# Kernel tuning notes

Measured on AMD Instinct MI355X. Metric: run time of the kernel, lower is better.

The kernel has to match this reference:

```python
import jax, jax.numpy as jnp
import numpy as np

B, T, F = 256, 2048, 20
H_NODES = 256


def _heaviside(x):
    # smooth heaviside approx used throughout the original module
    return (jnp.tanh(10.0 * x) + 1.0) * 0.5


def _evap(wu, wl, wd, pet):
    h = _heaviside
    et1 = h(wu - pet) * pet + h(pet - wu) * wu
    rp = h(pet - et1) * (pet - et1)  # h(-(pet-et1))*0 term vanishes
    et22 = h(rp - wl) * wl + h(wl - rp) * rp
    et2 = h(rp) * et22
    et33 = h(rp - et2 - wd) * wd + h(wd - (rp - et2)) * (rp - et2)
    et3 = h(rp - et2) * et33
    return et1, et2, et3


def _runoff(wu, wl, wd, p, wum, wlm, wdm, b, c):
    wum = wum * 19.9 + 0.1
    wlm = wlm * 30.0 + 60.0
    wdm = wdm * 60.0 + 60.0
    c = c * 0.19 + 0.01
    b = b * 0.3 + 0.1
    w_total = wum + wlm + wdm
    s = c * (wu / w_total) ** 2 + b * (wl / w_total) ** 2
    return _heaviside(p - s) * (p - s)


def _partition(runoff, k1, k2, k3):
    k1 = k1 * 0.69 + 0.01
    k2 = k2 * 0.69 + 0.01
    k3 = k3 * 0.89 + 0.01
    sr = k1 * runoff
    itf = k2 * (runoff - sr)
    bf = k3 * (runoff - sr - itf)
    return sr, itf, bf


def setup_inputs() -> dict:
    key = jax.random.key(0)
    ks = jax.random.split(key, 7)
    u = lambda k, shp: jax.random.uniform(k, shp, jnp.float32, -0.05, 0.05)
    inputs = jax.random.uniform(ks[0], (B, T, F), jnp.float32)
    return {
        "inputs": inputs,
        "w1": u(ks[1], (15, H_NODES)),
        "b1": jnp.zeros((H_NODES,), jnp.float32),
        "w2": u(ks[2], (H_NODES, 64)),
        "b2": jnp.zeros((64,), jnp.float32),
        "w3": u(ks[3], (64, 8)),
        "b3": jnp.zeros((8,), jnp.float32),
    }


def reference(inputs, w1, b1, w2, b2, w3, b3):
    pet = inputs[..., 0:1]
    tmean = inputs[..., 1:2]
    p = inputs[..., 2:3]
    attrs = inputs[..., 5:]  # [B,T,15]

    # static-attribute -> physical-parameter MLP
    h1 = jnp.tanh(attrs @ w1 + b1)
    h2 = jnp.tanh(h1 @ w2 + b2)
    params = jax.nn.sigmoid(h2 @ w3 + b3)  # [B,T,8]

    xs = jnp.concatenate([pet, p, tmean, params], axis=-1)  # [B,T,11]

    def step(state, x):
        wu, wl, wd = state[:, 0:1], state[:, 1:2], state[:, 2:3]
        pet_t, p_t = x[:, 0:1], x[:, 1:2]
        et1, et2, et3 = _evap(wu, wl, wd, pet_t)
        clip = lambda d: jnp.clip(d, -1e5, 1e5)
        wu_n = wu + clip(p_t - et1)
        wl_n = wl + clip(p_t - et1 - et2)
        wd_n = wd + clip(p_t - et1 - et2 - et3)
        ns = jnp.concatenate([wu_n, wl_n, wd_n], axis=1)  # [B,3]
        return ns, ns

    init = jnp.zeros((inputs.shape[0], 3), inputs.dtype)
    _, outs = jax.lax.scan(step, init, jnp.swapaxes(xs, 0, 1))  # [T,B,3]
    outputs = jnp.swapaxes(outs, 0, 1)  # [B,T,3]

    wu, wl, wd = outputs[..., 0:1], outputs[..., 1:2], outputs[..., 2:3]
    wum, wlm, wdm = params[..., 0:1], params[..., 1:2], params[..., 2:3]
    b, c = params[..., 3:4], params[..., 4:5]
    k1, k2, k3 = params[..., 5:6], params[..., 6:7], params[..., 7:8]

    et1, et2, et3 = _evap(wu, wl, wd, pet)
    # NOTE: original call() swaps (wl,wd) and (wlm,wdm) here - kept faithful
    runoff = _runoff(wu, wd, wl, p, wum, wdm, wlm, b, c)
    sr, itf, bf = _partition(runoff, k1, k2, k3)
    total_q = sr + itf * 0.5 + bf * 0.25  # flow routing
    return total_q  # [B,T,1]
```

## Files before the change

### kernel.cpp

```cpp
#include <hip/hip_runtime.h>

#define B_ 256
#define T_ 2048
#define F_ 20
#define NT (B_*T_)
#define CH 16
#define NCH (T_/CH)

typedef __bf16 bf16x8 __attribute__((ext_vector_type(8)));
typedef float  f32x4  __attribute__((ext_vector_type(4)));

__device__ __forceinline__ float ex2(float x){ return __builtin_amdgcn_exp2f(x); }
__device__ __forceinline__ float rcpf_(float x){ return __builtin_amdgcn_rcpf(x); }

#define K10F 28.853900817779268f
#define K1F   2.8853900817779268f
#define LOG2E 1.4426950408889634f

__device__ __forceinline__ float hside(float x){ return 1.0f - rcpf_(ex2(K10F*x) + 1.0f); }
__device__ __forceinline__ float tanh_f(float z){ return 1.0f - 2.0f*rcpf_(ex2(K1F*z) + 1.0f); }
__device__ __forceinline__ float sigmoid_f(float z){ return rcpf_(1.0f + ex2(-LOG2E*z)); }

__device__ __forceinline__ void lds_barrier(){
  asm volatile("s_waitcnt lgkmcnt(0)" ::: "memory");
  __builtin_amdgcn_s_barrier();
  asm volatile("" ::: "memory");
}


__global__ __launch_bounds__(256) void prep_kernel(const float* __restrict__ in,
                                                   float* __restrict__ ws){
  int r = blockIdx.x*256 + threadIdx.x;
  if (r >= NT) return;
  int b = r & (B_-1);
  int t = r >> 8;
  const float* src = in + ((size_t)b*T_ + t)*F_;
  ((float2*)ws)[r] = make_float2(src[0], src[2]);
}

__global__ __launch_bounds__(512) void fused_kernel(const float* __restrict__ in,
    const float* __restrict__ w1, const float* __restrict__ b1,
    const float* __restrict__ w2, const float* __restrict__ b2,
    const float* __restrict__ w3, const float* __restrict__ b3,
    float* __restrict__ ws){
  extern __shared__ char sm[];
  float* pk4 = ws + 4*(size_t)NT;

  if (blockIdx.x < 4) {
    asm volatile("s_setprio 3");
    const float2* pp2 = (const float2*)ws;
    float* wuT = ws + 2*(size_t)NT;
    float* wdT = ws + 3*(size_t)NT;
    float*  d1L = (float*)sm;
    float*  bsQ = (float*)(sm + 8192);
    float2* rhL = (float2*)(sm + 24576);
    float2* qbL = (float2*)(sm + 40960);

    int tid = threadIdx.x;
    int wv = tid >> 6, lane = tid & 63;
    int boff = blockIdx.x * 64;

    float wu = 0.0f, wl = 0.0f, wd = 0.0f;
    float2 buf[2][8];

    if (wv == 0){
      #pragma unroll
      for (int g = 0; g < 2; ++g)
        #pragma unroll
        for (int i = 0; i < 8; ++i)
          buf[g][i] = pp2[(g*8 + i)*B_ + boff + lane];
    }

    for (int it = 0; it < NCH + 3; ++it){
      if (wv == 0){
        if (it < NCH){
          int c = it, par = c & 1;
          #pragma unroll
          for (int g = 0; g < 2; ++g){
            #pragma unroll
            for (int i = 0; i < 8; ++i){
              int s = g*8 + i;
              float pet = buf[g][i].x, p = buf[g][i].y;
              float d  = wu - pet;
              float r1 = rcpf_(ex2(K10F*d) + 1.0f);
              float d1 = -d*r1;
              float base = (p - pet) + d1;
              wu += base;
              wuT[(c*CH + s)*B_ + boff + lane] = wu;
              d1L[par*(CH*64) + s*64 + lane] = d1;
              bsQ[(c&3)*(CH*64) + s*64 + lane] = base;
            }
            int cn = (c + 1 < NCH) ? c + 1 : c;
            #pragma unroll
            for (int i = 0; i < 8; ++i)
              buf[g][i] = pp2[(cn*CH + g*8 + i)*B_ + boff + lane];
          }
        }
      } else if (wv == 1){
        if (it >= 1 && it <= NCH){
          int c = it - 1, par = c & 1;
          #pragma unroll
          for (int s = 0; s < CH; ++s){
            float d1 = d1L[par*(CH*64) + s*64 + lane];
            float r2 = rcpf_(ex2(K10F*d1) + 1.0f);
            float rp = fmaf(-d1, r2, d1);
            float hrp = 1.0f - rcpf_(ex2(K10F*rp) + 1.0f);
            rhL[par*(CH*64) + s*64 + lane] = make_float2(rp, hrp);
          }
        }
      } else if (wv == 2){
        if (it >= 2 && it <= NCH + 1){
          int c = it - 2, par = c & 1;
          #pragma unroll
          for (int s = 0; s < CH; ++s){
            float2 rh  = rhL[par*(CH*64) + s*64 + lane];
            float base = bsQ[(c&3)*(CH*64) + s*64 + lane];
            float d2   = rh.x - wl;
            float r    = rcpf_(ex2(K10F*d2) + 1.0f);
            float et22 = fmaf(d2, r, wl);
            float et2  = rh.y * et22;
            float b2v  = base - et2;
            wl += b2v;
            qbL[par*(CH*64) + s*64 + lane] = make_float2(rh.x - et2, b2v);
          }
        }
      } else if (wv == 3){
        if (it >= 3){
          int c = it - 3, par = c & 1;
          #pragma unroll
          for (int s = 0; s < CH; ++s){
            float2 qb  = qbL[par*(CH*64) + s*64 + lane];
            float hqv  = 1.0f - rcpf_(ex2(K10F*qb.x) + 1.0f);
            float d3   = qb.x - wd;
            float r    = rcpf_(ex2(K10F*d3) + 1.0f);
            float et33 = fmaf(d3, r, wd);
            float et3  = hqv * et33;
            wd += qb.y - et3;
            wdT[(c*CH + s)*B_ + boff + lane] = wd;
          }
        }
      }
      lds_barrier();
    }
    return;
  }

  __bf16* w1f   = (__bf16*)sm;
  __bf16* w2f   = (__bf16*)(sm + 8192);
  float*  b1s   = (float*)(sm + 24576);
  float*  b2s   = (float*)(sm + 25600);
  float*  b3s   = (float*)(sm + 25856);
  __bf16* hbufA = (__bf16*)(sm + 25888);

  int tid  = threadIdx.x;
  int lane = tid & 63;
  int wv   = tid >> 6;
  int m    = lane & 15;
  int q    = lane >> 4;
  int r0   = (blockIdx.x - 4)*256 + wv*32;

  bf16x8 a1[2];
  #pragma unroll
  for (int u = 0; u < 2; ++u){
    int rowA = r0 + u*16 + m;
    int bA = rowA & (B_-1), tA = rowA >> 8;
    const float* ap = in + ((size_t)bA*T_ + tA)*F_ + 5;
    #pragma unroll
    for (int j = 0; j < 8; ++j){
      int k = q*8 + j;
      a1[u][j] = (__bf16)((k < 15) ? ap[k] : 0.0f);
    }
  }
  bf16x8 w3h[2], w3l[2];
  #pragma unroll
  for (int kb = 0; kb < 2; ++kb){
    #pragma unroll
    for (int j = 0; j < 8; ++j){
      float v = (m < 8) ? w3[(kb*32 + q*8 + j)*8 + m] : 0.0f;
      __bf16 hi = (__bf16)v;
      w3h[kb][j] = hi;
      w3l[kb][j] = (__bf16)(v - (float)hi);
    }
  }

  ((float4*)sm)[tid] = make_float4(0.0f, 0.0f, 0.0f, 0.0f);
  __syncthreads();
  for (int idx = tid; idx < 15*256; idx += 512){
    int k = idx >> 8, n = idx & 255;
    int ct = n >> 4;
    int l  = ((k>>3)*16) + (n & 15);
    int j  = k & 7;
    w1f[(ct*32 + l)*8 + j] = (__bf16)w1[idx];
  }
  for (int idx = tid; idx < 8192; idx += 512){
    int kk = idx >> 6, n = idx & 63;
    int kb2 = kk >> 5;
    int lq  = (kk >> 3) & 3;
    int j   = kk & 7;
    int ct  = n >> 4;
    int l   = lq*16 + (n & 15);
    w2f[((kb2*4 + ct)*64 + l)*8 + j] = (__bf16)w2[kk*64 + n];
  }
  if (tid < 256) b1s[tid] = b1[tid];
  if (tid < 64)  b2s[tid] = b2[tid];
  if (tid < 8)   b3s[tid] = b3[tid];
  __syncthreads();

  f32x4 zero4 = {0.0f, 0.0f, 0.0f, 0.0f};
  bf16x8 zero8;
  #pragma unroll
  for (int j = 0; j < 8; ++j) zero8[j] = (__bf16)0.0f;

  __bf16* hb = hbufA + wv*2304;
  f32x4 acc2[2][4] = {{zero4, zero4, zero4, zero4},
                      {zero4, zero4, zero4, zero4}};

  #pragma unroll
  for (int pc = 0; pc < 2; ++pc){
    if (pc == 1){
      __syncthreads();
      for (int idx = tid; idx < 8192; idx += 512){
        int kk = idx >> 6, n = idx & 63;
        int kb2 = kk >> 5;
        int lq  = (kk >> 3) & 3;
        int j   = kk & 7;
        int ct  = n >> 4;
        int l   = lq*16 + (n & 15);
        w2f[((kb2*4 + ct)*64 + l)*8 + j] = (__bf16)w2[(128 + kk)*64 + n];
      }
      __syncthreads();
    }
    #pragma unroll
    for (int ph = 0; ph < 2; ++ph){
      int p = pc*2 + ph;
      #pragma unroll
      for (int c4 = 0; c4 < 4; ++c4){
        int ct = p*4 + c4;
        bf16x8 bw = zero8;
        if (lane < 32) bw = *(const bf16x8*)&w1f[(ct*32 + lane)*8];
        int f = c4*16 + m;
        float bb = b1s[p*64 + f];
        #pragma unroll
        for (int u = 0; u < 2; ++u){
          f32x4 c1 = __builtin_amdgcn_mfma_f32_16x16x32_bf16(a1[u], bw, zero4, 0, 0, 0);
          #pragma unroll
          for (int i = 0; i < 4; ++i){
            float h = tanh_f(c1[i] + bb);
            hb[(u*16 + q*4 + i)*72 + f] = (__bf16)h;
          }
        }
      }
      #pragma unroll
      for (int kb = 0; kb < 2; ++kb){
        bf16x8 a2_0 = *(const bf16x8*)&hb[ m      *72 + kb*32 + q*8];
        bf16x8 a2_1 = *(const bf16x8*)&hb[(16 + m)*72 + kb*32 + q*8];
        #pragma unroll
        for (int ct = 0; ct < 4; ++ct){
          bf16x8 bw2 = *(const bf16x8*)&w2f[(((ph*2 + kb)*4 + ct)*64 + lane)*8];
          acc2[0][ct] = __builtin_amdgcn_mfma_f32_16x16x32_bf16(a2_0, bw2, acc2[0][ct], 0, 0, 0);
          acc2[1][ct] = __builtin_amdgcn_mfma_f32_16x16x32_bf16(a2_1, bw2, acc2[1][ct], 0, 0, 0);
        }
      }
    }
  }

  #pragma unroll
  for (int ct = 0; ct < 4; ++ct){
    int f = ct*16 + m;
    float bb = b2s[f];
    #pragma unroll
    for (int u = 0; u < 2; ++u)
      #pragma unroll
      for (int i = 0; i < 4; ++i){
        float h = tanh_f(acc2[u][ct][i] + bb);
        hb[(u*16 + q*4 + i)*72 + f] = (__bf16)h;
      }
  }

  f32x4 acc3[2] = {zero4, zero4};
  #pragma unroll
  for (int kb = 0; kb < 2; ++kb){
    bf16x8 a3_0 = *(const bf16x8*)&hb[ m      *72 + kb*32 + q*8];
    bf16x8 a3_1 = *(const bf16x8*)&hb[(16 + m)*72 + kb*32 + q*8];
    acc3[0] = __builtin_amdgcn_mfma_f32_16x16x32_bf16(a3_0, w3h[kb], acc3[0], 0, 0, 0);
    acc3[0] = __builtin_amdgcn_mfma_f32_16x16x32_bf16(a3_0, w3l[kb], acc3[0], 0, 0, 0);
    acc3[1] = __builtin_amdgcn_mfma_f32_16x16x32_bf16(a3_1, w3h[kb], acc3[1], 0, 0, 0);
    acc3[1] = __builtin_amdgcn_mfma_f32_16x16x32_bf16(a3_1, w3l[kb], acc3[1], 0, 0, 0);
  }

  float* hf = (float*)hb;
  if (m < 8){
    float bb3 = b3s[m];
    #pragma unroll
    for (int u = 0; u < 2; ++u)
      #pragma unroll
      for (int i = 0; i < 4; ++i)
        hf[(u*16 + q*4 + i)*9 + m] = sigmoid_f(acc3[u][i] + bb3);
  }
  if (lane < 32){
    const float* Pr = hf + lane*9;
    float P0=Pr[0], P1=Pr[1], P2=Pr[2], P3=Pr[3];
    float P4=Pr[4], P5=Pr[5], P6=Pr[6], P7=Pr[7];
    float wum = fmaf(P0, 19.9f, 0.1f);
    float wlm = fmaf(P2, 30.0f, 60.0f);
    float wdm = fmaf(P1, 60.0f, 60.0f);
    float wt  = wum + wlm + wdm;
    float rw  = 1.0f / wt;
    float cc  = fmaf(P4, 0.19f, 0.01f);
    float bc  = fmaf(P3, 0.30f, 0.10f);
    float A   = cc*rw*rw;
    float Bc  = bc*rw*rw;
    float k1  = fmaf(P5, 0.69f, 0.01f);
    float k2  = fmaf(P6, 0.69f, 0.01f);
    float k3  = fmaf(P7, 0.89f, 0.01f);
    float KP  = k1 + 0.5f*k2*(1.0f-k1) + 0.25f*k3*(1.0f-k1)*(1.0f-k2);
    *(float4*)&pk4[(size_t)(r0 + lane)*4] = make_float4(A, Bc, KP, 0.0f);
  }
}

__global__ __launch_bounds__(256) void final_kernel(const float* __restrict__ ws,
                                                    float* __restrict__ out){
  __shared__ float tile[64*65];
  int tb = blockIdx.x & 31;
  int bb = blockIdx.x >> 5;
  int t0 = tb*64, b0 = bb*64;
  int tid = threadIdx.x;
  const float2* pp2 = (const float2*)ws;
  const float* wuT  = ws + 2*(size_t)NT;
  const float* wdT  = ws + 3*(size_t)NT;
  const float* pk4  = ws + 4*(size_t)NT;

  #pragma unroll
  for (int k = 0; k < 16; ++k){
    int idx = k*256 + tid;
    int tl = idx >> 6, bl = idx & 63;
    int r = (t0 + tl)*B_ + b0 + bl;
    float p  = pp2[r].y;
    float wu = wuT[r], wd = wdT[r];
    float4 k4 = *(const float4*)&pk4[(size_t)r*4];
    float ps = p - k4.x*wu*wu - k4.y*wd*wd;
    float runoff = hside(ps)*ps;
    tile[bl*65 + tl] = k4.z * runoff;
  }
  __syncthreads();
  #pragma unroll
  for (int k = 0; k < 16; ++k){
    int idx = k*256 + tid;
    int tl2 = idx & 63, bl2 = idx >> 6;
    out[(size_t)(b0 + bl2)*T_ + t0 + tl2] = tile[bl2*65 + tl2];
  }
}

extern "C" void kernel_launch(void* const* d_in, const int* in_sizes, int n_in,
                              void* d_out, int out_size, void* d_ws, size_t ws_size,
                              hipStream_t stream) {
  const float* in = (const float*)d_in[0];
  const float* w1 = (const float*)d_in[1];
  const float* b1 = (const float*)d_in[2];
  const float* w2 = (const float*)d_in[3];
  const float* b2 = (const float*)d_in[4];
  const float* w3 = (const float*)d_in[5];
  const float* b3 = (const float*)d_in[6];
  float* out = (float*)d_out;
  float* ws  = (float*)d_ws;

  prep_kernel <<<NT/256,     256, 0,     stream>>>(in, ws);
  fused_kernel<<<NT/256 + 4, 512, 62752, stream>>>(in, w1, b1, w2, b2, w3, b3, ws);
  final_kernel<<<128,        256, 0,     stream>>>(ws, out);
}
```

Baseline: 215.4 us.

## Fold input gather into scan blocks via LDS streaming and shrink final tiles

```diff
diff --git a/kernel.cpp b/kernel.cpp
--- a/kernel.cpp
+++ b/kernel.cpp
@@ -27,16 +27,6 @@
   asm volatile("" ::: "memory");
 }
 
-
-__global__ __launch_bounds__(256) void prep_kernel(const float* __restrict__ in,
-                                                   float* __restrict__ ws){
-  int r = blockIdx.x*256 + threadIdx.x;
-  if (r >= NT) return;
-  int b = r & (B_-1);
-  int t = r >> 8;
-  const float* src = in + ((size_t)b*T_ + t)*F_;
-  ((float2*)ws)[r] = make_float2(src[0], src[2]);
-}
 
 __global__ __launch_bounds__(512) void fused_kernel(const float* __restrict__ in,
     const float* __restrict__ w1, const float* __restrict__ b1,
@@ -48,55 +38,63 @@
 
   if (blockIdx.x < 4) {
     asm volatile("s_setprio 3");
-    const float2* pp2 = (const float2*)ws;
+    float* pT  = ws;
     float* wuT = ws + 2*(size_t)NT;
     float* wdT = ws + 3*(size_t)NT;
     float*  d1L = (float*)sm;
     float*  bsQ = (float*)(sm + 8192);
     float2* rhL = (float2*)(sm + 24576);
     float2* qbL = (float2*)(sm + 40960);
+    float2* ppL = (float2*)(sm + 57344);
 
     int tid = threadIdx.x;
     int wv = tid >> 6, lane = tid & 63;
     int boff = blockIdx.x * 64;
+    const float* bp = in + (size_t)(boff + lane)*T_*F_;
 
     float wu = 0.0f, wl = 0.0f, wd = 0.0f;
-    float2 buf[2][8];
-
-    if (wv == 0){
-      #pragma unroll
-      for (int g = 0; g < 2; ++g)
-        #pragma unroll
-        for (int i = 0; i < 8; ++i)
-          buf[g][i] = pp2[(g*8 + i)*B_ + boff + lane];
-    }
+
+    if (wv == 1){
+      float4 v[CH];
+      #pragma unroll
+      for (int s = 0; s < CH; ++s)
+        v[s] = *(const float4*)(bp + (size_t)s*F_);
+      #pragma unroll
+      for (int s = 0; s < CH; ++s){
+        ppL[s*64 + lane] = make_float2(v[s].x, v[s].z);
+        pT[s*B_ + boff + lane] = v[s].z;
+      }
+    }
+    lds_barrier();
 
     for (int it = 0; it < NCH + 3; ++it){
       if (wv == 0){
         if (it < NCH){
           int c = it, par = c & 1;
           #pragma unroll
-          for (int g = 0; g < 2; ++g){
-            #pragma unroll
-            for (int i = 0; i < 8; ++i){
-              int s = g*8 + i;
-              float pet = buf[g][i].x, p = buf[g][i].y;
-              float d  = wu - pet;
-              float r1 = rcpf_(ex2(K10F*d) + 1.0f);
-              float d1 = -d*r1;
-              float base = (p - pet) + d1;
-              wu += base;
-              wuT[(c*CH + s)*B_ + boff + lane] = wu;
-              d1L[par*(CH*64) + s*64 + lane] = d1;
-              bsQ[(c&3)*(CH*64) + s*64 + lane] = base;
-            }
-            int cn = (c + 1 < NCH) ? c + 1 : c;
-            #pragma unroll
-            for (int i = 0; i < 8; ++i)
-              buf[g][i] = pp2[(cn*CH + g*8 + i)*B_ + boff + lane];
+          for (int s = 0; s < CH; ++s){
+            float2 pp = ppL[(par*CH + s)*64 + lane];
+            float pet = pp.x, p = pp.y;
+            float d  = wu - pet;
+            float r1 = rcpf_(ex2(K10F*d) + 1.0f);
+            float d1 = -d*r1;
+            float base = (p - pet) + d1;
+            wu += base;
+            wuT[(c*CH + s)*B_ + boff + lane] = wu;
+            d1L[par*(CH*64) + s*64 + lane] = d1;
+            bsQ[(c&3)*(CH*64) + s*64 + lane] = base;
           }
         }
       } else if (wv == 1){
+        int cs = it + 1;
+        bool doStream = (cs < NCH);
+        float4 v[CH];
+        if (doStream){
+          const float* cp = bp + (size_t)cs*CH*F_;
+          #pragma unroll
+          for (int s = 0; s < CH; ++s)
+            v[s] = *(const float4*)(cp + (size_t)s*F_);
+        }
         if (it >= 1 && it <= NCH){
           int c = it - 1, par = c & 1;
           #pragma unroll
@@ -106,6 +104,14 @@
             float rp = fmaf(-d1, r2, d1);
             float hrp = 1.0f - rcpf_(ex2(K10F*rp) + 1.0f);
             rhL[par*(CH*64) + s*64 + lane] = make_float2(rp, hrp);
+          }
+        }
+        if (doStream){
+          int ps_ = cs & 1;
+          #pragma unroll
+          for (int s = 0; s < CH; ++s){
+            ppL[(ps_*CH + s)*64 + lane] = make_float2(v[s].x, v[s].z);
+            pT[(cs*CH + s)*B_ + boff + lane] = v[s].z;
           }
         }
       } else if (wv == 2){
@@ -320,34 +326,34 @@
 
 __global__ __launch_bounds__(256) void final_kernel(const float* __restrict__ ws,
                                                     float* __restrict__ out){
-  __shared__ float tile[64*65];
-  int tb = blockIdx.x & 31;
-  int bb = blockIdx.x >> 5;
-  int t0 = tb*64, b0 = bb*64;
+  __shared__ float tile[64*17];
+  int tb = blockIdx.x >> 2;
+  int bb = blockIdx.x & 3;
+  int t0 = tb*16, b0 = bb*64;
   int tid = threadIdx.x;
-  const float2* pp2 = (const float2*)ws;
+  const float* pT   = ws;
   const float* wuT  = ws + 2*(size_t)NT;
   const float* wdT  = ws + 3*(size_t)NT;
   const float* pk4  = ws + 4*(size_t)NT;
 
   #pragma unroll
-  for (int k = 0; k < 16; ++k){
+  for (int k = 0; k < 4; ++k){
     int idx = k*256 + tid;
     int tl = idx >> 6, bl = idx & 63;
     int r = (t0 + tl)*B_ + b0 + bl;
-    float p  = pp2[r].y;
+    float p  = pT[r];
     float wu = wuT[r], wd = wdT[r];
     float4 k4 = *(const float4*)&pk4[(size_t)r*4];
     float ps = p - k4.x*wu*wu - k4.y*wd*wd;
     float runoff = hside(ps)*ps;
-    tile[bl*65 + tl] = k4.z * runoff;
+    tile[bl*17 + tl] = k4.z * runoff;
   }
   __syncthreads();
   #pragma unroll
-  for (int k = 0; k < 16; ++k){
+  for (int k = 0; k < 4; ++k){
     int idx = k*256 + tid;
-    int tl2 = idx & 63, bl2 = idx >> 6;
-    out[(size_t)(b0 + bl2)*T_ + t0 + tl2] = tile[bl2*65 + tl2];
+    int tl2 = idx & 15, bl2 = idx >> 4;
+    out[(size_t)(b0 + bl2)*T_ + t0 + tl2] = tile[bl2*17 + tl2];
   }
 }
 
@@ -364,7 +370,13 @@
   float* out = (float*)d_out;
   float* ws  = (float*)d_ws;
 
-  prep_kernel <<<NT/256,     256, 0,     stream>>>(in, ws);
-  fused_kernel<<<NT/256 + 4, 512, 62752, stream>>>(in, w1, b1, w2, b2, w3, b3, ws);
-  final_kernel<<<128,        256, 0,     stream>>>(ws, out);
+  static bool attr_set = false;
+  if (!attr_set){
+    hipFuncSetAttribute((const void*)fused_kernel,
+                        hipFuncAttributeMaxDynamicSharedMemorySize, 73728);
+    attr_set = true;
+  }
+
+  fused_kernel<<<NT/256 + 4, 512, 73728, stream>>>(in, w1, b1, w2, b2, w3, b3, ws);
+  final_kernel<<<512,        256, 0,     stream>>>(ws, out);
 }
```

New measurement: 277.6 us. 1.29x slower.
